# Performance work log

Measured on AMD Instinct MI355X. Metric: run time of the kernel, lower is better.

## Reference

```python
import jax, jax.numpy as jnp
import numpy as np


def _gcn_layer(h, src, dst, W, b, norm_src, norm_dst, n_nodes):
    # DGL GraphConv with norm='both': D_out^{-1/2} -> sum-aggregate -> D_in^{-1/2} -> XW + b
    m = (h * norm_src[:, None])[src]                       # [E, d] gather
    agg = jax.ops.segment_sum(m, dst, num_segments=n_nodes)  # [N, d] scatter-add
    return agg * norm_dst[:, None] @ W + b


def reference(features, src, dst, W1, b1, W2, b2):
    n_nodes = features.shape[0]
    ones = jnp.ones(src.shape[0], dtype=features.dtype)
    deg_out = jax.ops.segment_sum(ones, src, num_segments=n_nodes)
    deg_in = jax.ops.segment_sum(ones, dst, num_segments=n_nodes)
    # DGL clamps degrees to min 1 before the -1/2 power
    norm_src = jnp.clip(deg_out, 1.0, None) ** -0.5
    norm_dst = jnp.clip(deg_in, 1.0, None) ** -0.5

    h = jax.nn.relu(_gcn_layer(features, src, dst, W1, b1, norm_src, norm_dst, n_nodes))
    h = jax.nn.relu(_gcn_layer(h, src, dst, W2, b2, norm_src, norm_dst, n_nodes))
    return h


def setup_inputs() -> dict:
    key = jax.random.key(0)
    k1, k2, k3, k4, k5 = jax.random.split(key, 5)
    N, E, D = 50000, 600000, 128
    scale = 1.0 / np.sqrt(D)
    return {
        "features": jax.random.normal(k1, (N, D), dtype=jnp.float32),
        "src": jax.random.randint(k2, (E,), 0, N, dtype=jnp.int32),
        "dst": jax.random.randint(k3, (E,), 0, N, dtype=jnp.int32),
        "W1": jax.random.normal(k4, (D, D), dtype=jnp.float32) * scale,
        "b1": jnp.zeros((D,), dtype=jnp.float32),
        "W2": jax.random.normal(k5, (D, D), dtype=jnp.float32) * scale,
        "b2": jnp.zeros((D,), dtype=jnp.float32),
    }
```

## Files before the change

kernel.cpp:

```cpp
#include <hip/hip_runtime.h>

#define DIM 128
#define HBD 64
#define HBS 64
#define HWORDS 25088
#define WSTR 136

typedef __attribute__((ext_vector_type(8))) short b8;
typedef __attribute__((ext_vector_type(4))) float f4;
typedef __attribute__((ext_vector_type(8))) unsigned short u16x8;

static __device__ __forceinline__ unsigned short f2bf(float f) {
    unsigned u = __float_as_uint(f);
    u += 0x7fffu + ((u >> 16) & 1u);
    return (unsigned short)(u >> 16);
}
static __device__ __forceinline__ float bf2f(unsigned short b) {
    return __uint_as_float((unsigned)b << 16);
}

__global__ __launch_bounds__(1024) void k_hist(const int* __restrict__ src,
                                               const int* __restrict__ dst,
                                               unsigned short* __restrict__ local,
                                               unsigned* __restrict__ hist_in,
                                               unsigned* __restrict__ hist_out,
                                               const float* __restrict__ feat,
                                               unsigned short* __restrict__ fbf,
                                               const float* __restrict__ W1,
                                               const float* __restrict__ W2,
                                               unsigned short* __restrict__ w1hi,
                                               unsigned short* __restrict__ w1lo,
                                               unsigned short* __restrict__ w2hi,
                                               unsigned short* __restrict__ w2lo,
                                               int* __restrict__ scan_aux,
                                               int E, int W2p, int slice_d, int slice_s,
                                               int n4) {
    const int t = threadIdx.x;
    const int bx = blockIdx.x;
    if (bx < HBD + HBS) {
        __shared__ unsigned h[HWORDS];
        const bool is_dst = bx < HBD;
        const int b = is_dst ? bx : bx - HBD;
        const int slice = is_dst ? slice_d : slice_s;
        const int e0 = b * slice;
        const int e1 = min(e0 + slice, E);
        const int W4 = W2p >> 2;
        uint4* h4 = (uint4*)h;

        for (int w = t; w < W4; w += 1024) h4[w] = make_uint4(0u, 0u, 0u, 0u);
        __syncthreads();

        if (is_dst) {
            int e = e0 + t;
            int d = (e < e1) ? dst[e] : 0;
            while (e < e1) {
                int en = e + 1024;
                int dn = (en < e1) ? dst[en] : 0;
                unsigned sh = (unsigned)(d & 1) * 16u;
                unsigned old = atomicAdd(&h[d >> 1], 1u << sh);
                local[e] = (unsigned short)((old >> sh) & 0xffffu);
                e = en; d = dn;
            }
        } else {
            int e = e0 + t;
            int s = (e < e1) ? src[e] : 0;
            while (e < e1) {
                int en = e + 1024;
                int sn = (en < e1) ? src[en] : 0;
                atomicAdd(&h[s >> 1], 1u << ((unsigned)(s & 1) * 16u));
                e = en; s = sn;
            }
        }
        __syncthreads();

        uint4* o = (uint4*)((is_dst ? hist_in : hist_out) + (size_t)b * W2p);
        for (int w = t; w < W4; w += 1024) o[w] = h4[w];
    } else if (bx < HBD + HBS + 2) {
        int b = bx - (HBD + HBS);
        if (b == 0 && t < 256) scan_aux[t] = 0;
        const float* W = b ? W2 : W1;
        unsigned short* Hi = b ? w2hi : w1hi;
        unsigned short* Lo = b ? w2lo : w1lo;
        for (int e = t; e < DIM * DIM; e += 1024) {
            int k = e >> 7, c = e & 127;
            float w = W[e];
            unsigned short hi = f2bf(w);
            unsigned short lo = f2bf(w - bf2f(hi));
            Hi[c * DIM + k] = hi;
            Lo[c * DIM + k] = lo;
        }
    } else {
        int i = (bx - (HBD + HBS + 2)) * 1024 + t;
        if (i < n4) {
            float4 v = ((const float4*)feat)[i];
            ushort4 o;
            o.x = f2bf(v.x); o.y = f2bf(v.y);
            o.z = f2bf(v.z); o.w = f2bf(v.w);
            ((ushort4*)fbf)[i] = o;
        }
    }
}

__global__ __launch_bounds__(256) void k_scan(unsigned* __restrict__ hist_in,
                                              const unsigned* __restrict__ hist_out,
                                              int* __restrict__ partials,
                                              int* __restrict__ flags,
                                              int* __restrict__ row_off,
                                              float* __restrict__ norm_src,
                                              float* __restrict__ norm_dst,
                                              int W2, int W2p, int N) {
    __shared__ int wsum[4];
    __shared__ int wbase[4];
    __shared__ int psum[4];
    __shared__ int base_s;
    const int t = threadIdx.x;
    const int b = blockIdx.x;
    const int w = b * 256 + t;
    const int lane = t & 63, wave = t >> 6;

    unsigned run = 0, run2 = 0;
    if (w < W2) {
        unsigned* p = hist_in + w;
        #pragma unroll 8
        for (int i = 0; i < HBD; ++i) {
            unsigned x = *p;
            *p = run;
            run += x;
            p += W2p;
        }
        const unsigned* q = hist_out + w;
        #pragma unroll 8
        for (int i = 0; i < HBS; ++i) { run2 += *q; q += W2p; }
    }
    const int n0 = w * 2, n1 = n0 + 1;
    const int lo = (int)(run & 0xffffu), hi = (int)(run >> 16);
    const int s = (w < W2) ? (lo + ((n1 < N) ? hi : 0)) : 0;

    int x = s;
    #pragma unroll
    for (int off = 1; off < 64; off <<= 1) {
        int y = __shfl_up(x, off, 64);
        if (lane >= off) x += y;
    }
    if (lane == 63) wsum[wave] = x;
    __syncthreads();
    if (t == 0) {
        int acc = 0;
        #pragma unroll
        for (int i = 0; i < 4; ++i) { int v = wsum[i]; wbase[i] = acc; acc += v; }
        partials[b] = acc;
        __threadfence();
        atomicExch(&flags[b], 1);
    }
    __syncthreads();

    int pre = 0;
    if (t < b) {
        while (atomicAdd(&flags[t], 0) == 0) { __builtin_amdgcn_s_sleep(2); }
        pre = atomicAdd(&partials[t], 0);
    }
    #pragma unroll
    for (int off = 32; off > 0; off >>= 1) pre += __shfl_down(pre, off, 64);
    if (lane == 0) psum[wave] = pre;
    __syncthreads();
    if (t == 0) base_s = psum[0] + psum[1] + psum[2] + psum[3];
    __syncthreads();
    const int B = base_s;

    if (w < W2) {
        int tb = B + wbase[wave] + (x - s);
        row_off[n0] = tb;
        int dlo = lo < 1 ? 1 : lo;
        norm_dst[n0] = rsqrtf((float)dlo);
        int o0 = (int)(run2 & 0xffffu); if (o0 < 1) o0 = 1;
        norm_src[n0] = rsqrtf((float)o0);
        if (n1 < N) {
            row_off[n1] = tb + lo;
            int dhi = hi < 1 ? 1 : hi;
            norm_dst[n1] = rsqrtf((float)dhi);
            int o1 = (int)(run2 >> 16); if (o1 < 1) o1 = 1;
            norm_src[n1] = rsqrtf((float)o1);
            if (n1 == N - 1) row_off[N] = tb + lo + hi;
        } else if (n0 == N - 1) {
            row_off[N] = tb + lo;
        }
    }
}

__global__ __launch_bounds__(256) void k_fill(const int* __restrict__ src,
                                              const int* __restrict__ dst,
                                              const int* __restrict__ row_off,
                                              const unsigned short* __restrict__ local,
                                              const unsigned* __restrict__ hist_in,
                                              int* __restrict__ csr_src,
                                              int E, int W2p, int slice) {
    int e = blockIdx.x * 256 + threadIdx.x;
    if (e >= E) return;
    int d = dst[e];
    int b = e / slice;
    unsigned sh = (unsigned)(d & 1) * 16u;
    unsigned bo = (hist_in[(size_t)b * W2p + (d >> 1)] >> sh) & 0xffffu;
    csr_src[row_off[d] + (int)bo + (int)local[e]] = src[e];
}

__global__ __launch_bounds__(256) void k_edge_pass_fb(const int* __restrict__ src,
                                                      const int* __restrict__ dst,
                                                      int* __restrict__ deg_out,
                                                      int* __restrict__ cnt,
                                                      int* __restrict__ local_fb, int E) {
    int e = blockIdx.x * 256 + threadIdx.x;
    if (e < E) {
        atomicAdd(&deg_out[src[e]], 1);
        local_fb[e] = atomicAdd(&cnt[dst[e]], 1);
    }
}

__global__ __launch_bounds__(256) void k_block_reduce(const int* __restrict__ deg,
                                                      int* __restrict__ bsum, int N) {
    __shared__ int wsum[4];
    int i = blockIdx.x * 256 + threadIdx.x;
    int x = (i < N) ? deg[i] : 0;
    #pragma unroll
    for (int off = 32; off > 0; off >>= 1) x += __shfl_down(x, off, 64);
    int lane = threadIdx.x & 63, wave = threadIdx.x >> 6;
    if (lane == 0) wsum[wave] = x;
    __syncthreads();
    if (threadIdx.x == 0) bsum[blockIdx.x] = wsum[0] + wsum[1] + wsum[2] + wsum[3];
}

__global__ __launch_bounds__(256) void k_scan_final(const int* __restrict__ cnt,
                                                    const int* __restrict__ deg_out,
                                                    const int* __restrict__ bsum,
                                                    int* __restrict__ row_off,
                                                    float* __restrict__ norm_src,
                                                    float* __restrict__ norm_dst, int N) {
    __shared__ int wsum[4];
    __shared__ int base_s;
    const int t = threadIdx.x;
    const int lane = t & 63, wave = t >> 6;

    int pre = 0;
    for (int i = t; i < blockIdx.x; i += 256) pre += bsum[i];
    #pragma unroll
    for (int off = 32; off > 0; off >>= 1) pre += __shfl_down(pre, off, 64);
    if (lane == 0) wsum[wave] = pre;
    __syncthreads();
    if (t == 0) base_s = wsum[0] + wsum[1] + wsum[2] + wsum[3];
    __syncthreads();
    const int bpre_v = base_s;

    int i = blockIdx.x * 256 + t;
    int x = (i < N) ? cnt[i] : 0;
    int orig = x;
    #pragma unroll
    for (int off = 1; off < 64; off <<= 1) {
        int y = __shfl_up(x, off, 64);
        if (lane >= off) x += y;
    }
    if (lane == 63) wsum[wave] = x;
    __syncthreads();
    if (t == 0) {
        int s = 0;
        for (int w = 0; w < 4; ++w) { int tt = wsum[w]; wsum[w] = s; s += tt; }
    }
    __syncthreads();
    x += wsum[wave] + bpre_v;
    if (i < N) {
        row_off[i] = x - orig;
        int di = orig < 1 ? 1 : orig;
        norm_dst[i] = rsqrtf((float)di);
        int dov = deg_out[i]; if (dov < 1) dov = 1;
        norm_src[i] = rsqrtf((float)dov);
    }
    if (i == N - 1) row_off[N] = x;
}

__global__ __launch_bounds__(256) void k_fill_cast_prep_fb(
        const int* __restrict__ src, const int* __restrict__ dst,
        const int* __restrict__ row_off,
        const int* __restrict__ local_fb,
        int* __restrict__ csr_src,
        const float* __restrict__ feat,
        unsigned short* __restrict__ fbf,
        const float* __restrict__ W1, const float* __restrict__ W2,
        unsigned short* __restrict__ w1hi, unsigned short* __restrict__ w1lo,
        unsigned short* __restrict__ w2hi, unsigned short* __restrict__ w2lo,
        int E, int eb, int cb, int pb, int n4) {
    int bx = blockIdx.x;
    if (bx < eb) {
        int e = bx * 256 + threadIdx.x;
        if (e < E) {
            int d = dst[e];
            csr_src[row_off[d] + local_fb[e]] = src[e];
        }
    } else if (bx < eb + cb) {
        int i = (bx - eb) * 256 + threadIdx.x;
        if (i < n4) {
            float4 v = ((const float4*)feat)[i];
            ushort4 o;
            o.x = f2bf(v.x); o.y = f2bf(v.y);
            o.z = f2bf(v.z); o.w = f2bf(v.w);
            ((ushort4*)fbf)[i] = o;
        }
    } else {
        int b = bx - eb - cb;
        const float* W; unsigned short *Hi, *Lo;
        if (b < pb) { W = W1; Hi = w1hi; Lo = w1lo; } else { W = W2; Hi = w2hi; Lo = w2lo; b -= pb; }
        int e = b * 256 + threadIdx.x;
        if (e < DIM * DIM) {
            int k = e >> 7, c = e & 127;
            float w = W[e];
            unsigned short hi = f2bf(w);
            unsigned short lo = f2bf(w - bf2f(hi));
            Hi[c * DIM + k] = hi;
            Lo[c * DIM + k] = lo;
        }
    }
}

template<bool SCALE>
__global__ __launch_bounds__(256) void k_spmm(const unsigned short* __restrict__ hb,
                                              const int* __restrict__ csr_src,
                                              const int* __restrict__ row_off,
                                              const float* __restrict__ norm_src,
                                              const float* __restrict__ norm_dst,
                                              unsigned short* __restrict__ aggbf, int N) {
    int t = blockIdx.x * 256 + threadIdx.x;
    int node = t >> 4;
    int lane = t & 15;
    if (node >= N) return;
    int beg = row_off[node], end = row_off[node + 1];
    float a0[8] = {0.f, 0.f, 0.f, 0.f, 0.f, 0.f, 0.f, 0.f};
    float a1[8] = {0.f, 0.f, 0.f, 0.f, 0.f, 0.f, 0.f, 0.f};
    int i = beg;
    int s0 = 0, s1 = 0, s2 = 0, s3 = 0;
    if (i + 4 <= end) {
        s0 = csr_src[i]; s1 = csr_src[i + 1]; s2 = csr_src[i + 2]; s3 = csr_src[i + 3];
    }
    while (i + 4 <= end) {
        u16x8 u0 = *((const u16x8*)(hb + (size_t)s0 * DIM) + lane);
        u16x8 u1 = *((const u16x8*)(hb + (size_t)s1 * DIM) + lane);
        u16x8 u2 = *((const u16x8*)(hb + (size_t)s2 * DIM) + lane);
        u16x8 u3 = *((const u16x8*)(hb + (size_t)s3 * DIM) + lane);
        float ns0 = 1.f, ns1 = 1.f, ns2 = 1.f, ns3 = 1.f;
        if (SCALE) {
            ns0 = norm_src[s0]; ns1 = norm_src[s1];
            ns2 = norm_src[s2]; ns3 = norm_src[s3];
        }
        int i2 = i + 4;
        if (i2 + 4 <= end) {
            s0 = csr_src[i2]; s1 = csr_src[i2 + 1]; s2 = csr_src[i2 + 2]; s3 = csr_src[i2 + 3];
        }
        #pragma unroll
        for (int j = 0; j < 8; ++j) {
            if (SCALE) {
                a0[j] = fmaf(bf2f(u0[j]), ns0, a0[j]);
                a1[j] = fmaf(bf2f(u1[j]), ns1, a1[j]);
                a0[j] = fmaf(bf2f(u2[j]), ns2, a0[j]);
                a1[j] = fmaf(bf2f(u3[j]), ns3, a1[j]);
            } else {
                a0[j] += bf2f(u0[j]);
                a1[j] += bf2f(u1[j]);
                a0[j] += bf2f(u2[j]);
                a1[j] += bf2f(u3[j]);
            }
        }
        i = i2;
    }
    for (; i < end; ++i) {
        int s = csr_src[i];
        float ns = SCALE ? norm_src[s] : 1.f;
        u16x8 u = *((const u16x8*)(hb + (size_t)s * DIM) + lane);
        #pragma unroll
        for (int j = 0; j < 8; ++j) {
            if (SCALE) a0[j] = fmaf(bf2f(u[j]), ns, a0[j]);
            else       a0[j] += bf2f(u[j]);
        }
    }
    float nd = norm_dst[node];
    u16x8 o;
    #pragma unroll
    for (int j = 0; j < 8; ++j) o[j] = f2bf((a0[j] + a1[j]) * nd);
    *((u16x8*)(aggbf + (size_t)node * DIM) + lane) = o;
}

__global__ __launch_bounds__(256, 2) void k_gemm_mfma(
        const unsigned short* __restrict__ A,
        const unsigned short* __restrict__ Wt_hi,
        const unsigned short* __restrict__ Wt_lo,
        const float* __restrict__ bias,
        const float* __restrict__ postscale,
        float* __restrict__ outf, unsigned short* __restrict__ outbf, int N) {
    __shared__ unsigned short WH[DIM * WSTR];
    __shared__ unsigned short WL[DIM * WSTR];

    const int t = threadIdx.x;
    #pragma unroll
    for (int i = 0; i < 8; ++i) {
        int e = (t + i * 256) * 8;
        int c = e >> 7, k = e & 127;
        *(float4*)(WH + c * WSTR + k) = *(const float4*)(Wt_hi + e);
        *(float4*)(WL + c * WSTR + k) = *(const float4*)(Wt_lo + e);
    }
    __syncthreads();

    const int wv = t >> 6;
    const int l = t & 63;
    const int m = l & 15;
    const int quad = l >> 4;
    const int row_t0 = blockIdx.x * 128 + wv * 32;

    f4 acc[2][8];
    #pragma unroll
    for (int rt = 0; rt < 2; ++rt)
        #pragma unroll
        for (int ct = 0; ct < 8; ++ct)
            acc[rt][ct] = (f4){0.f, 0.f, 0.f, 0.f};

    int r0 = row_t0 + m;      if (r0 >= N) r0 = N - 1;
    int r1 = row_t0 + 16 + m; if (r1 >= N) r1 = N - 1;

    #pragma unroll
    for (int ks = 0; ks < 4; ++ks) {
        int koff = ks * 32 + quad * 8;
        b8 a0 = *(const b8*)(A + (size_t)r0 * DIM + koff);
        b8 a1 = *(const b8*)(A + (size_t)r1 * DIM + koff);
        #pragma unroll
        for (int ct = 0; ct < 8; ++ct) {
            int c = ct * 16 + m;
            b8 bh = *(const b8*)(WH + c * WSTR + koff);
            b8 bl = *(const b8*)(WL + c * WSTR + koff);
            acc[0][ct] = __builtin_amdgcn_mfma_f32_16x16x32_bf16(a0, bh, acc[0][ct], 0, 0, 0);
            acc[0][ct] = __builtin_amdgcn_mfma_f32_16x16x32_bf16(a0, bl, acc[0][ct], 0, 0, 0);
            acc[1][ct] = __builtin_amdgcn_mfma_f32_16x16x32_bf16(a1, bh, acc[1][ct], 0, 0, 0);
            acc[1][ct] = __builtin_amdgcn_mfma_f32_16x16x32_bf16(a1, bl, acc[1][ct], 0, 0, 0);
        }
    }

    #pragma unroll
    for (int rt = 0; rt < 2; ++rt) {
        int rowb = row_t0 + rt * 16 + quad * 4;
        #pragma unroll
        for (int r = 0; r < 4; ++r) {
            int gr = rowb + r;
            if (gr < N) {
                float s = postscale ? postscale[gr] : 1.f;
                #pragma unroll
                for (int ct = 0; ct < 8; ++ct) {
                    int col = ct * 16 + m;
                    float v = fmaxf(acc[rt][ct][r] + bias[col], 0.f) * s;
                    if (outbf) outbf[(size_t)gr * DIM + col] = f2bf(v);
                    else       outf[(size_t)gr * DIM + col] = v;
                }
            }
        }
    }
}

static inline size_t align_up(size_t x, size_t a) { return (x + a - 1) & ~(a - 1); }

extern "C" void kernel_launch(void* const* d_in, const int* in_sizes, int n_in,
                              void* d_out, int out_size, void* d_ws, size_t ws_size,
                              hipStream_t stream) {
    const float* features = (const float*)d_in[0];
    const int*   src      = (const int*)d_in[1];
    const int*   dst      = (const int*)d_in[2];
    const float* W1       = (const float*)d_in[3];
    const float* b1       = (const float*)d_in[4];
    const float* W2       = (const float*)d_in[5];
    const float* b2       = (const float*)d_in[6];
    float* out = (float*)d_out;

    const int N = in_sizes[0] / DIM;
    const int E = in_sizes[1];
    const int B = (N + 255) / 256;
    const int W2w = (N + 1) >> 1;
    const int W2p = (W2w + 3) & ~3;
    const int slice_d = (E + HBD - 1) / HBD;
    const int slice_s = (E + HBS - 1) / HBS;
    const int cs_blocks = (W2w + 255) / 256;

    size_t nodeb = align_up((size_t)N * 4, 256);
    char* p = (char*)d_ws;
    int*   deg_out  = (int*)p;                      p += nodeb;
    int*   cnt      = (int*)p;                      p += nodeb;
    float* norm_src = (float*)p;                    p += nodeb;
    float* norm_dst = (float*)p;                    p += nodeb;
    int*   row_off  = (int*)p;                      p += align_up((size_t)(N + 1) * 4, 256);
    int*   scan_aux = (int*)p;                      p += align_up((size_t)(B + 256) * 4, 256);
    int*   csr_src  = (int*)p;                      p += align_up((size_t)E * 4, 256);
    char*  big      = p;                            p += 2 * (size_t)N * DIM * 4;
    unsigned short* w1hi = (unsigned short*)p;      p += (size_t)DIM * DIM * 2;
    unsigned short* w1lo = (unsigned short*)p;      p += (size_t)DIM * DIM * 2;
    unsigned short* w2hi = (unsigned short*)p;      p += (size_t)DIM * DIM * 2;
    unsigned short* w2lo = (unsigned short*)p;      p += (size_t)DIM * DIM * 2;
    unsigned short* aggbf = (unsigned short*)big;
    unsigned short* h1bf  = (unsigned short*)(big + (size_t)N * DIM * 2);
    unsigned short* fbf   = (unsigned short*)(big + 3 * (size_t)N * DIM * 2);
    char* ap = big;
    unsigned short* local = (unsigned short*)ap;    ap += align_up((size_t)E * 2, 256);
    unsigned* hist_in  = (unsigned*)ap;             ap += (size_t)HBD * W2p * 4;
    unsigned* hist_out = (unsigned*)ap;             ap += (size_t)HBS * W2p * 4;
    int* local_fb = (int*)big;
    int* partials = scan_aux;
    int* flags    = scan_aux + 128;
    int* bsum     = scan_aux;

    const int edge_blocks = (E + 255) / 256;
    const int spmm_blocks = (int)(((size_t)N * 16 + 255) / 256);
    const int gemm_blocks = (N + 127) / 128;
    const int n4 = N * (DIM / 4);
    const int cast_blocks1k = (n4 + 1023) / 1024;
    const int mega_blocks = HBD + HBS + 2 + cast_blocks1k;

    const bool fast = (W2p <= HWORDS) && (cs_blocks <= 256) &&
        (align_up((size_t)E * 2, 256) + (size_t)(HBD + HBS) * W2p * 4
            <= 3 * (size_t)N * DIM * 2);

    if (fast) {
        k_hist<<<mega_blocks, 1024, 0, stream>>>(src, dst, local, hist_in, hist_out,
                                                 features, fbf, W1, W2,
                                                 w1hi, w1lo, w2hi, w2lo, scan_aux,
                                                 E, W2p, slice_d, slice_s, n4);
        k_scan<<<cs_blocks, 256, 0, stream>>>(hist_in, hist_out, partials, flags,
                                              row_off, norm_src, norm_dst, W2w, W2p, N);
        k_fill<<<edge_blocks, 256, 0, stream>>>(src, dst, row_off, local, hist_in,
                                                csr_src, E, W2p, slice_d);
    } else {
        const int cast_blocks = (n4 + 255) / 256;
        const int prep_blocks = (DIM * DIM + 255) / 256;
        hipMemsetAsync(deg_out, 0, nodeb * 2, stream);
        k_edge_pass_fb<<<edge_blocks, 256, 0, stream>>>(src, dst, deg_out, cnt, local_fb, E);
        k_block_reduce<<<B, 256, 0, stream>>>(cnt, bsum, N);
        k_scan_final<<<B, 256, 0, stream>>>(cnt, deg_out, bsum, row_off, norm_src, norm_dst, N);
        k_fill_cast_prep_fb<<<edge_blocks + cast_blocks + 2 * prep_blocks, 256, 0, stream>>>(
            src, dst, row_off, local_fb, csr_src, features, fbf,
            W1, W2, w1hi, w1lo, w2hi, w2lo,
            E, edge_blocks, cast_blocks, prep_blocks, n4);
    }

    k_spmm<true><<<spmm_blocks, 256, 0, stream>>>(fbf, csr_src, row_off, norm_src,
                                                  norm_dst, aggbf, N);
    k_gemm_mfma<<<gemm_blocks, 256, 0, stream>>>(aggbf, w1hi, w1lo, b1, norm_src,
                                                 (float*)nullptr, h1bf, N);

    k_spmm<false><<<spmm_blocks, 256, 0, stream>>>(h1bf, csr_src, row_off,
                                                   (const float*)nullptr,
                                                   norm_dst, aggbf, N);
    k_gemm_mfma<<<gemm_blocks, 256, 0, stream>>>(aggbf, w2hi, w2lo, b2,
                                                 (const float*)nullptr,
                                                 out, (unsigned short*)nullptr, N);
}
```

Baseline: 218.3 us.

## Fuse SpMM aggregation and MFMA GEMM into one per-layer kernel

Each GCN layer is now a single 1024-thread kernel. It gathers neighbor rows for 256 nodes into an LDS tile and then runs the bf16 hi/lo MFMA GEMM straight from LDS. This removes the intermediate aggregated-feature buffer's global write and read, plus two kernel launches. In exchange, the large LDS footprint (weights plus the A tile) allows about one block per CU. Only about 196 blocks are launched, fewer than the CU count, which limits occupancy for the latency-bound gather. The software prefetch of CSR indices is also dropped.

New measurement: 217.9 us. No clear change (-0.2%).

```diff
diff --git a/kernel.cpp b/kernel.cpp
--- a/kernel.cpp
+++ b/kernel.cpp
@@ -319,73 +319,12 @@
 }
 
 template<bool SCALE>
-__global__ __launch_bounds__(256) void k_spmm(const unsigned short* __restrict__ hb,
-                                              const int* __restrict__ csr_src,
-                                              const int* __restrict__ row_off,
-                                              const float* __restrict__ norm_src,
-                                              const float* __restrict__ norm_dst,
-                                              unsigned short* __restrict__ aggbf, int N) {
-    int t = blockIdx.x * 256 + threadIdx.x;
-    int node = t >> 4;
-    int lane = t & 15;
-    if (node >= N) return;
-    int beg = row_off[node], end = row_off[node + 1];
-    float a0[8] = {0.f, 0.f, 0.f, 0.f, 0.f, 0.f, 0.f, 0.f};
-    float a1[8] = {0.f, 0.f, 0.f, 0.f, 0.f, 0.f, 0.f, 0.f};
-    int i = beg;
-    int s0 = 0, s1 = 0, s2 = 0, s3 = 0;
-    if (i + 4 <= end) {
-        s0 = csr_src[i]; s1 = csr_src[i + 1]; s2 = csr_src[i + 2]; s3 = csr_src[i + 3];
-    }
-    while (i + 4 <= end) {
-        u16x8 u0 = *((const u16x8*)(hb + (size_t)s0 * DIM) + lane);
-        u16x8 u1 = *((const u16x8*)(hb + (size_t)s1 * DIM) + lane);
-        u16x8 u2 = *((const u16x8*)(hb + (size_t)s2 * DIM) + lane);
-        u16x8 u3 = *((const u16x8*)(hb + (size_t)s3 * DIM) + lane);
-        float ns0 = 1.f, ns1 = 1.f, ns2 = 1.f, ns3 = 1.f;
-        if (SCALE) {
-            ns0 = norm_src[s0]; ns1 = norm_src[s1];
-            ns2 = norm_src[s2]; ns3 = norm_src[s3];
-        }
-        int i2 = i + 4;
-        if (i2 + 4 <= end) {
-            s0 = csr_src[i2]; s1 = csr_src[i2 + 1]; s2 = csr_src[i2 + 2]; s3 = csr_src[i2 + 3];
-        }
-        #pragma unroll
-        for (int j = 0; j < 8; ++j) {
-            if (SCALE) {
-                a0[j] = fmaf(bf2f(u0[j]), ns0, a0[j]);
-                a1[j] = fmaf(bf2f(u1[j]), ns1, a1[j]);
-                a0[j] = fmaf(bf2f(u2[j]), ns2, a0[j]);
-                a1[j] = fmaf(bf2f(u3[j]), ns3, a1[j]);
-            } else {
-                a0[j] += bf2f(u0[j]);
-                a1[j] += bf2f(u1[j]);
-                a0[j] += bf2f(u2[j]);
-                a1[j] += bf2f(u3[j]);
-            }
-        }
-        i = i2;
-    }
-    for (; i < end; ++i) {
-        int s = csr_src[i];
-        float ns = SCALE ? norm_src[s] : 1.f;
-        u16x8 u = *((const u16x8*)(hb + (size_t)s * DIM) + lane);
-        #pragma unroll
-        for (int j = 0; j < 8; ++j) {
-            if (SCALE) a0[j] = fmaf(bf2f(u[j]), ns, a0[j]);
-            else       a0[j] += bf2f(u[j]);
-        }
-    }
-    float nd = norm_dst[node];
-    u16x8 o;
-    #pragma unroll
-    for (int j = 0; j < 8; ++j) o[j] = f2bf((a0[j] + a1[j]) * nd);
-    *((u16x8*)(aggbf + (size_t)node * DIM) + lane) = o;
-}
-
-__global__ __launch_bounds__(256, 2) void k_gemm_mfma(
-        const unsigned short* __restrict__ A,
+__global__ __launch_bounds__(1024, 4) void k_layer(
+        const unsigned short* __restrict__ hb,
+        const int* __restrict__ csr_src,
+        const int* __restrict__ row_off,
+        const float* __restrict__ norm_src,
+        const float* __restrict__ norm_dst,
         const unsigned short* __restrict__ Wt_hi,
         const unsigned short* __restrict__ Wt_lo,
         const float* __restrict__ bias,
@@ -393,14 +332,71 @@
         float* __restrict__ outf, unsigned short* __restrict__ outbf, int N) {
     __shared__ unsigned short WH[DIM * WSTR];
     __shared__ unsigned short WL[DIM * WSTR];
+    __shared__ unsigned short AT[256 * WSTR];
 
     const int t = threadIdx.x;
     #pragma unroll
-    for (int i = 0; i < 8; ++i) {
-        int e = (t + i * 256) * 8;
+    for (int i = 0; i < 2; ++i) {
+        int e = (t + i * 1024) * 8;
         int c = e >> 7, k = e & 127;
         *(float4*)(WH + c * WSTR + k) = *(const float4*)(Wt_hi + e);
         *(float4*)(WL + c * WSTR + k) = *(const float4*)(Wt_lo + e);
+    }
+
+    const int nb = blockIdx.x * 256;
+    const int lane16 = t & 15;
+    #pragma unroll 1
+    for (int p = 0; p < 4; ++p) {
+        int nl = p * 64 + (t >> 4);
+        int node = nb + nl;
+        if (node < N) {
+            int beg = row_off[node], end = row_off[node + 1];
+            float a0[8] = {0.f, 0.f, 0.f, 0.f, 0.f, 0.f, 0.f, 0.f};
+            float a1[8] = {0.f, 0.f, 0.f, 0.f, 0.f, 0.f, 0.f, 0.f};
+            int i = beg;
+            for (; i + 4 <= end; i += 4) {
+                int s0 = csr_src[i], s1 = csr_src[i + 1];
+                int s2 = csr_src[i + 2], s3 = csr_src[i + 3];
+                u16x8 u0 = *((const u16x8*)(hb + (size_t)s0 * DIM) + lane16);
+                u16x8 u1 = *((const u16x8*)(hb + (size_t)s1 * DIM) + lane16);
+                u16x8 u2 = *((const u16x8*)(hb + (size_t)s2 * DIM) + lane16);
+                u16x8 u3 = *((const u16x8*)(hb + (size_t)s3 * DIM) + lane16);
+                float ns0 = 1.f, ns1 = 1.f, ns2 = 1.f, ns3 = 1.f;
+                if (SCALE) {
+                    ns0 = norm_src[s0]; ns1 = norm_src[s1];
+                    ns2 = norm_src[s2]; ns3 = norm_src[s3];
+                }
+                #pragma unroll
+                for (int j = 0; j < 8; ++j) {
+                    if (SCALE) {
+                        a0[j] = fmaf(bf2f(u0[j]), ns0, a0[j]);
+                        a1[j] = fmaf(bf2f(u1[j]), ns1, a1[j]);
+                        a0[j] = fmaf(bf2f(u2[j]), ns2, a0[j]);
+                        a1[j] = fmaf(bf2f(u3[j]), ns3, a1[j]);
+                    } else {
+                        a0[j] += bf2f(u0[j]);
+                        a1[j] += bf2f(u1[j]);
+                        a0[j] += bf2f(u2[j]);
+                        a1[j] += bf2f(u3[j]);
+                    }
+                }
+            }
+            for (; i < end; ++i) {
+                int s = csr_src[i];
+                float ns = SCALE ? norm_src[s] : 1.f;
+                u16x8 u = *((const u16x8*)(hb + (size_t)s * DIM) + lane16);
+                #pragma unroll
+                for (int j = 0; j < 8; ++j) {
+                    if (SCALE) a0[j] = fmaf(bf2f(u[j]), ns, a0[j]);
+                    else       a0[j] += bf2f(u[j]);
+                }
+            }
+            float nd = norm_dst[node];
+            u16x8 o;
+            #pragma unroll
+            for (int j = 0; j < 8; ++j) o[j] = f2bf((a0[j] + a1[j]) * nd);
+            *(u16x8*)(AT + nl * WSTR + lane16 * 8) = o;
+        }
     }
     __syncthreads();
 
@@ -408,50 +404,37 @@
     const int l = t & 63;
     const int m = l & 15;
     const int quad = l >> 4;
-    const int row_t0 = blockIdx.x * 128 + wv * 32;
-
-    f4 acc[2][8];
-    #pragma unroll
-    for (int rt = 0; rt < 2; ++rt)
-        #pragma unroll
-        for (int ct = 0; ct < 8; ++ct)
-            acc[rt][ct] = (f4){0.f, 0.f, 0.f, 0.f};
-
-    int r0 = row_t0 + m;      if (r0 >= N) r0 = N - 1;
-    int r1 = row_t0 + 16 + m; if (r1 >= N) r1 = N - 1;
+
+    f4 acc[8];
+    #pragma unroll
+    for (int ct = 0; ct < 8; ++ct) acc[ct] = (f4){0.f, 0.f, 0.f, 0.f};
 
     #pragma unroll
     for (int ks = 0; ks < 4; ++ks) {
         int koff = ks * 32 + quad * 8;
-        b8 a0 = *(const b8*)(A + (size_t)r0 * DIM + koff);
-        b8 a1 = *(const b8*)(A + (size_t)r1 * DIM + koff);
+        b8 a = *(const b8*)(AT + (wv * 16 + m) * WSTR + koff);
         #pragma unroll
         for (int ct = 0; ct < 8; ++ct) {
             int c = ct * 16 + m;
             b8 bh = *(const b8*)(WH + c * WSTR + koff);
             b8 bl = *(const b8*)(WL + c * WSTR + koff);
-            acc[0][ct] = __builtin_amdgcn_mfma_f32_16x16x32_bf16(a0, bh, acc[0][ct], 0, 0, 0);
-            acc[0][ct] = __builtin_amdgcn_mfma_f32_16x16x32_bf16(a0, bl, acc[0][ct], 0, 0, 0);
-            acc[1][ct] = __builtin_amdgcn_mfma_f32_16x16x32_bf16(a1, bh, acc[1][ct], 0, 0, 0);
-            acc[1][ct] = __builtin_amdgcn_mfma_f32_16x16x32_bf16(a1, bl, acc[1][ct], 0, 0, 0);
-        }
-    }
-
-    #pragma unroll
-    for (int rt = 0; rt < 2; ++rt) {
-        int rowb = row_t0 + rt * 16 + quad * 4;
-        #pragma unroll
-        for (int r = 0; r < 4; ++r) {
-            int gr = rowb + r;
-            if (gr < N) {
-                float s = postscale ? postscale[gr] : 1.f;
-                #pragma unroll
-                for (int ct = 0; ct < 8; ++ct) {
-                    int col = ct * 16 + m;
-                    float v = fmaxf(acc[rt][ct][r] + bias[col], 0.f) * s;
-                    if (outbf) outbf[(size_t)gr * DIM + col] = f2bf(v);
-                    else       outf[(size_t)gr * DIM + col] = v;
-                }
+            acc[ct] = __builtin_amdgcn_mfma_f32_16x16x32_bf16(a, bh, acc[ct], 0, 0, 0);
+            acc[ct] = __builtin_amdgcn_mfma_f32_16x16x32_bf16(a, bl, acc[ct], 0, 0, 0);
+        }
+    }
+
+    int rowb = nb + wv * 16 + quad * 4;
+    #pragma unroll
+    for (int r = 0; r < 4; ++r) {
+        int gr = rowb + r;
+        if (gr < N) {
+            float s = postscale ? postscale[gr] : 1.f;
+            #pragma unroll
+            for (int ct = 0; ct < 8; ++ct) {
+                int col = ct * 16 + m;
+                float v = fmaxf(acc[ct][r] + bias[col], 0.f) * s;
+                if (outbf) outbf[(size_t)gr * DIM + col] = f2bf(v);
+                else       outf[(size_t)gr * DIM + col] = v;
             }
         }
     }
@@ -494,7 +477,6 @@
     unsigned short* w1lo = (unsigned short*)p;      p += (size_t)DIM * DIM * 2;
     unsigned short* w2hi = (unsigned short*)p;      p += (size_t)DIM * DIM * 2;
     unsigned short* w2lo = (unsigned short*)p;      p += (size_t)DIM * DIM * 2;
-    unsigned short* aggbf = (unsigned short*)big;
     unsigned short* h1bf  = (unsigned short*)(big + (size_t)N * DIM * 2);
     unsigned short* fbf   = (unsigned short*)(big + 3 * (size_t)N * DIM * 2);
     char* ap = big;
@@ -507,8 +489,7 @@
     int* bsum     = scan_aux;
 
     const int edge_blocks = (E + 255) / 256;
-    const int spmm_blocks = (int)(((size_t)N * 16 + 255) / 256);
-    const int gemm_blocks = (N + 127) / 128;
+    const int layer_blocks = (N + 255) / 256;
     const int n4 = N * (DIM / 4);
     const int cast_blocks1k = (n4 + 1023) / 1024;
     const int mega_blocks = HBD + HBS + 2 + cast_blocks1k;
@@ -539,15 +520,11 @@
             E, edge_blocks, cast_blocks, prep_blocks, n4);
     }
 
-    k_spmm<true><<<spmm_blocks, 256, 0, stream>>>(fbf, csr_src, row_off, norm_src,
-                                                  norm_dst, aggbf, N);
-    k_gemm_mfma<<<gemm_blocks, 256, 0, stream>>>(aggbf, w1hi, w1lo, b1, norm_src,
-                                                 (float*)nullptr, h1bf, N);
-
-    k_spmm<false><<<spmm_blocks, 256, 0, stream>>>(h1bf, csr_src, row_off,
-                                                   (const float*)nullptr,
-                                                   norm_dst, aggbf, N);
-    k_gemm_mfma<<<gemm_blocks, 256, 0, stream>>>(aggbf, w2hi, w2lo, b2,
-                                                 (const float*)nullptr,
-                                                 out, (unsigned short*)nullptr, N);
-}
+    k_layer<true><<<layer_blocks, 1024, 0, stream>>>(
+        fbf, csr_src, row_off, norm_src, norm_dst,
+        w1hi, w1lo, b1, norm_src, (float*)nullptr, h1bf, N);
+
+    k_layer<false><<<layer_blocks, 1024, 0, stream>>>(
+        h1bf, csr_src, row_off, (const float*)nullptr, norm_dst,
+        w2hi, w2lo, b2, (const float*)nullptr, out, (unsigned short*)nullptr, N);
+}
```
